# Performance work log

Hardware: AMD Instinct MI355X
Metric: run time of the kernel (lower is better)

The kernel has to match this reference:

```python
import jax, jax.numpy as jnp
from jax import lax
import numpy as np

B, S, E, H, V = 16, 512, 300, 512, 10000


def setup_inputs() -> dict:
    key = jax.random.key(0)
    ks = jax.random.split(key, 7)
    sE = 1.0 / np.sqrt(H)  # torch nn.RNN init scale U(-1/sqrt(H), 1/sqrt(H)); randn*scale is fine for a numeric baseline
    return {
        "x": jax.random.normal(ks[0], (B, S, E), dtype=jnp.float32),
        "W_ih": jax.random.normal(ks[1], (H, E), dtype=jnp.float32) * sE,
        "W_hh": jax.random.normal(ks[2], (H, H), dtype=jnp.float32) * sE,
        "b_ih": jax.random.normal(ks[3], (H,), dtype=jnp.float32) * sE,
        "b_hh": jax.random.normal(ks[4], (H,), dtype=jnp.float32) * sE,
        "W_fc": jax.random.normal(ks[5], (V, H), dtype=jnp.float32) * sE,
        "b_fc": jax.random.normal(ks[6], (V,), dtype=jnp.float32) * sE,
    }


def reference(x, W_ih, W_hh, b_ih, b_hh, W_fc, b_fc):
    # Precompute the input projection for all timesteps: [B,S,H]
    xw = jnp.einsum("bse,he->bsh", x, W_ih) + b_ih + b_hh

    def step(h, xt):
        # h: [B,H], xt: [B,H]
        h = jnp.tanh(xt + h @ W_hh.T)
        return h, h

    h0 = jnp.zeros((x.shape[0], W_hh.shape[0]), dtype=x.dtype)
    _, hs = lax.scan(step, h0, jnp.swapaxes(xw, 0, 1))  # hs: [S,B,H]
    hs = jnp.swapaxes(hs, 0, 1)  # [B,S,H]
    logits = jnp.einsum("bsh,vh->bsv", hs, W_fc) + b_fc  # [B,S,V]
    # Faithful to source: Softmax(dim=1) -> over the SEQUENCE axis
    return jax.nn.softmax(logits, axis=1)
```

## Files before the change

### kernel.cpp

```cpp
#include <hip/hip_runtime.h>
#include <hip/hip_bf16.h>
#include <math.h>

#define B_ 16
#define S_ 512
#define E_ 300
#define H_ 512
#define V_ 10000
#define BS_ (B_ * S_)

#define NSL 16
#define JPB (H_ / NSL)
#define NBLK (B_ * NSL)

typedef __attribute__((ext_vector_type(4))) float f32x4;
typedef __attribute__((ext_vector_type(8))) short bf16x8;
typedef unsigned long long u64;

#define PART_WORDS (4 * B_ * H_)

__global__ __launch_bounds__(256) void k0_init(u64* __restrict__ part) {
  const int idx = blockIdx.x * 256 + threadIdx.x;
  part[idx] = 0xFFFFFFFF00000000ull;
}

__global__ __launch_bounds__(256) void k1_xw(const float* __restrict__ x,
                                             const float* __restrict__ W_ih,
                                             const float* __restrict__ b_ih,
                                             const float* __restrict__ b_hh,
                                             float* __restrict__ xw) {
  __shared__ float As[64][156];
  __shared__ float Ws[64][156];
  const int row0 = blockIdx.x * 64;
  const int col0 = blockIdx.y * 64;
  const int tid = threadIdx.x;
  const int ty = tid >> 4, tx = tid & 15;
  float acc[4][4];
#pragma unroll
  for (int ii = 0; ii < 4; ++ii)
#pragma unroll
    for (int jj = 0; jj < 4; ++jj) acc[ii][jj] = 0.f;

  for (int idx = tid; idx < 64 * 38; idx += 256) {
    const int r = idx / 38, e4 = idx - r * 38;
    *(float4*)&As[r][e4 * 4] =
        *(const float4*)&x[(size_t)(row0 + r) * E_ + e4 * 4];
    *(float4*)&Ws[r][e4 * 4] =
        *(const float4*)&W_ih[(size_t)(col0 + r) * E_ + e4 * 4];
  }
  __syncthreads();
#pragma unroll 2
  for (int e4 = 0; e4 < 38; ++e4) {
    f32x4 a[4], w[4];
#pragma unroll
    for (int ii = 0; ii < 4; ++ii)
      a[ii] = *(const f32x4*)&As[ty + 16 * ii][e4 * 4];
#pragma unroll
    for (int jj = 0; jj < 4; ++jj)
      w[jj] = *(const f32x4*)&Ws[tx + 16 * jj][e4 * 4];
#pragma unroll
    for (int ii = 0; ii < 4; ++ii)
#pragma unroll
      for (int jj = 0; jj < 4; ++jj) {
        const f32x4 p = a[ii] * w[jj];
        acc[ii][jj] += p.x + p.y + p.z + p.w;
      }
  }
  __syncthreads();

  for (int idx = tid; idx < 64 * 37; idx += 256) {
    const int r = idx / 37, e4 = idx - r * 37;
    *(float4*)&As[r][e4 * 4] =
        *(const float4*)&x[(size_t)(row0 + r) * E_ + 152 + e4 * 4];
    *(float4*)&Ws[r][e4 * 4] =
        *(const float4*)&W_ih[(size_t)(col0 + r) * E_ + 152 + e4 * 4];
  }
  __syncthreads();
#pragma unroll 2
  for (int e4 = 0; e4 < 37; ++e4) {
    f32x4 a[4], w[4];
#pragma unroll
    for (int ii = 0; ii < 4; ++ii)
      a[ii] = *(const f32x4*)&As[ty + 16 * ii][e4 * 4];
#pragma unroll
    for (int jj = 0; jj < 4; ++jj)
      w[jj] = *(const f32x4*)&Ws[tx + 16 * jj][e4 * 4];
#pragma unroll
    for (int ii = 0; ii < 4; ++ii)
#pragma unroll
      for (int jj = 0; jj < 4; ++jj) {
        const f32x4 p = a[ii] * w[jj];
        acc[ii][jj] += p.x + p.y + p.z + p.w;
      }
  }

#pragma unroll
  for (int jj = 0; jj < 4; ++jj) {
    const int h = col0 + tx + 16 * jj;
    const float bb = b_ih[h] + b_hh[h];
#pragma unroll
    for (int ii = 0; ii < 4; ++ii)
      xw[(size_t)(row0 + ty + 16 * ii) * H_ + h] = acc[ii][jj] + bb;
  }
}

__device__ __forceinline__ u64 pload(const u64* p) {
  return __hip_atomic_load(p, __ATOMIC_RELAXED, __HIP_MEMORY_SCOPE_AGENT);
}
__device__ __forceinline__ u64 load_sc0(const u64* p) {
  u64 r;
  asm volatile("global_load_dwordx2 %0, %1, off sc0\n\ts_waitcnt vmcnt(0)"
               : "=v"(r) : "v"(p) : "memory");
  return r;
}
__device__ __forceinline__ void store_sc0(u64* p, u64 v) {
  asm volatile("global_store_dwordx2 %0, %1, off sc0" :: "v"(p), "v"(v)
               : "memory");
}

__global__ __launch_bounds__(512) void k2_scan(
    const float* __restrict__ xw, const float* __restrict__ W_hh,
    float* __restrict__ hs, u64* __restrict__ part) {
  const int b = blockIdx.x & 15;
  const int g = blockIdx.x >> 4;
  const int tid = threadIdx.x;
  const int j = tid >> 4;
  const int q = tid & 15;
  const int jg = g * JPB + j;

  __shared__ f32x4 Wp[8 * 512];
  __shared__ f32x4 hp4[2][128];

  {
    const float* wrow = &W_hh[(size_t)jg * H_ + q * 32];
#pragma unroll
    for (int i4 = 0; i4 < 8; ++i4)
      Wp[i4 * 512 + tid] = *(const f32x4*)&wrow[i4 * 4];
  }
  if (tid < 128) hp4[0][tid] = (f32x4)0.f;

  u64* const pf = part + (size_t)b * H_;
  u64* const ps = part + (size_t)(2 * B_ + b) * H_;
  const int kk = ((tid & 63) >> 2) * 32 + (tid >> 6) * 4 + (tid & 3);
  bool fast = true;

  float xwv = xw[(size_t)b * S_ * H_ + jg];
  __syncthreads();

  for (int t = 0; t < S_; ++t) {
    const int cur = t & 1;
    f32x4 a4 = (f32x4)0.f;
#pragma unroll
    for (int i4 = 0; i4 < 8; ++i4) {
      const f32x4 wv = Wp[i4 * 512 + tid];
      const f32x4 hv = hp4[cur][i4 * 16 + q];
      a4 += wv * hv;
    }
    float acc = a4.x + a4.y + a4.z + a4.w;
    acc += __shfl_xor(acc, 1);
    acc += __shfl_xor(acc, 2);
    acc += __shfl_xor(acc, 4);
    acc += __shfl_xor(acc, 8);

    if (q == 0) {
      const float hn = tanhf(xwv + acc);
      const u64 pk =
          ((u64)(unsigned)t << 32) | (u64)(unsigned)__float_as_uint(hn);
      store_sc0(&pf[(size_t)cur * (B_ * H_) + jg], pk);
      __hip_atomic_store(&ps[(size_t)cur * (B_ * H_) + jg], pk,
                         __ATOMIC_RELAXED, __HIP_MEMORY_SCOPE_AGENT);
      hs[((size_t)b * S_ + t) * H_ + jg] = hn;
    }
    const int tn = (t + 1 < S_) ? t + 1 : t;
    const float xw_next = xw[((size_t)b * S_ + tn) * H_ + jg];

    if (t + 1 < S_) {
      u64 v = 0;
      bool got = false;
      const u64* fw = &pf[(size_t)cur * (B_ * H_) + kk];
      if (fast) {
        for (int it = 0; it < 64; ++it) {
          v = load_sc0(fw);
          if ((unsigned)(v >> 32) == (unsigned)t) { got = true; break; }
        }
        if (!got) fast = false;
      }
      if (!got) {
        const u64* sw = &ps[(size_t)cur * (B_ * H_) + kk];
        v = pload(sw);
        while ((unsigned)(v >> 32) != (unsigned)t) v = pload(sw);
      }
      ((float*)&hp4[cur ^ 1][0])[tid] = __uint_as_float((unsigned)v);
    }
    xwv = xw_next;
    __syncthreads();
  }
}

__device__ __forceinline__ unsigned short bf16_rtn(float f) {
  unsigned u = __float_as_uint(f);
  return (unsigned short)((u + 0x7FFFu + ((u >> 16) & 1u)) >> 16);
}
__global__ __launch_bounds__(256) void k5_split(const float* __restrict__ src,
                                                unsigned short* __restrict__ hi,
                                                unsigned short* __restrict__ lo,
                                                int n4) {
  const int i = blockIdx.x * 256 + threadIdx.x;
  if (i >= n4) return;
  const float4 f = *(const float4*)&src[i * 4];
  unsigned short h[4], l[4];
  const float ff[4] = {f.x, f.y, f.z, f.w};
#pragma unroll
  for (int k = 0; k < 4; ++k) {
    h[k] = bf16_rtn(ff[k]);
    const float fh = __uint_as_float((unsigned)h[k] << 16);
    l[k] = bf16_rtn(ff[k] - fh);
  }
  *(ushort4*)&hi[i * 4] = make_ushort4(h[0], h[1], h[2], h[3]);
  *(ushort4*)&lo[i * 4] = make_ushort4(l[0], l[1], l[2], l[3]);
}

__global__ __launch_bounds__(256) void k5_cast(const float* __restrict__ src,
                                               unsigned short* __restrict__ dst,
                                               int n4) {
  const int i = blockIdx.x * 256 + threadIdx.x;
  if (i >= n4) return;
  const float4 f = *(const float4*)&src[i * 4];
  *(ushort4*)&dst[i * 4] = make_ushort4(bf16_rtn(f.x), bf16_rtn(f.y),
                                        bf16_rtn(f.z), bf16_rtn(f.w));
}

__global__ __launch_bounds__(256) void k3_logits(
    const unsigned short* __restrict__ Abg, const unsigned short* __restrict__ Bhg,
    const unsigned short* __restrict__ Blg, const float* __restrict__ b_fc,
    float* __restrict__ out, float2* __restrict__ pstats) {
  __shared__ unsigned short Ab[2][128 * 32];
  __shared__ unsigned short Bh[2][128 * 32];
  __shared__ unsigned short Bl[2][128 * 32];
  __shared__ float2 sstat[2][2][4][16];
  const int m0 = blockIdx.x * 128;
  const int n0 = blockIdx.y * 128;
  const int tid = threadIdx.x;
  const int lane = tid & 63;
  const int wave = tid >> 6;
  const int wm = wave >> 1, wn = wave & 1;
  const int lr = lane & 15;
  const int lg = lane >> 4;
  const int cxr = (lg ^ (lr & 3)) * 8;
  const int lrow = lane >> 2;
  const int lchunk = (lane & 3) ^ (lrow & 3);

  const unsigned short* src[6];
  unsigned short* d0[6];
  unsigned short* d1[6];
#pragma unroll
  for (int t = 0; t < 6; ++t) {
    const int id = wave * 6 + t;
    const int arr = id >> 3;
    const int c16 = id & 7;
    const int r = c16 * 16 + lrow;
    const int grow = (arr == 0) ? (m0 + r) : min(n0 + r, V_ - 1);
    const unsigned short* g = (arr == 0) ? Abg : (arr == 1) ? Bhg : Blg;
    src[t] = g + (size_t)grow * H_ + lchunk * 8;
    unsigned short* l0 = (arr == 0) ? Ab[0] : (arr == 1) ? Bh[0] : Bl[0];
    unsigned short* l1 = (arr == 0) ? Ab[1] : (arr == 1) ? Bh[1] : Bl[1];
    d0[t] = l0 + c16 * 512;
    d1[t] = l1 + c16 * 512;
  }

  f32x4 acc[4][4];
#pragma unroll
  for (int mi = 0; mi < 4; ++mi)
#pragma unroll
    for (int ni = 0; ni < 4; ++ni) acc[mi][ni] = (f32x4)0.0f;

  auto STAGE0 = [&](int k0) {
#pragma unroll
    for (int t = 0; t < 6; ++t)
      __builtin_amdgcn_global_load_lds(
          (const __attribute__((address_space(1))) void*)(src[t] + k0),
          (__attribute__((address_space(3))) void*)d0[t], 16, 0, 0);
  };
  auto STAGE1 = [&](int k0) {
#pragma unroll
    for (int t = 0; t < 6; ++t)
      __builtin_amdgcn_global_load_lds(
          (const __attribute__((address_space(1))) void*)(src[t] + k0),
          (__attribute__((address_space(3))) void*)d1[t], 16, 0, 0);
  };
  auto COMPUTE = [&](int buf) {
    bf16x8 ab[4], bh[4], bl[4];
#pragma unroll
    for (int i = 0; i < 4; ++i) {
      ab[i] = *(const bf16x8*)&Ab[buf][(wm * 64 + i * 16 + lr) * 32 + cxr];
      bh[i] = *(const bf16x8*)&Bh[buf][(wn * 64 + i * 16 + lr) * 32 + cxr];
      bl[i] = *(const bf16x8*)&Bl[buf][(wn * 64 + i * 16 + lr) * 32 + cxr];
    }
#pragma unroll
    for (int mi = 0; mi < 4; ++mi)
#pragma unroll
      for (int ni = 0; ni < 4; ++ni) {
        acc[mi][ni] = __builtin_amdgcn_mfma_f32_16x16x32_bf16(
            ab[mi], bh[ni], acc[mi][ni], 0, 0, 0);
        acc[mi][ni] = __builtin_amdgcn_mfma_f32_16x16x32_bf16(
            ab[mi], bl[ni], acc[mi][ni], 0, 0, 0);
      }
  };

  STAGE0(0);
  __syncthreads();
  for (int kt = 0; kt < 16; kt += 2) {
    STAGE1((kt + 1) * 32);
    COMPUTE(0);
    __syncthreads();
    if (kt + 2 < 16) STAGE0((kt + 2) * 32);
    COMPUTE(1);
    __syncthreads();
  }

#pragma unroll
  for (int ni = 0; ni < 4; ++ni) {
    const int v = n0 + wn * 64 + ni * 16 + lr;
    if (v >= V_) continue;
    const float bias = b_fc[v];
#pragma unroll
    for (int mi = 0; mi < 4; ++mi) {
      const int mrow = m0 + wm * 64 + mi * 16 + lg * 4;
#pragma unroll
      for (int r = 0; r < 4; ++r)
        out[(size_t)(mrow + r) * V_ + v] = acc[mi][ni][r] + bias;
    }
  }

  float pm[4], psum[4];
#pragma unroll
  for (int ni = 0; ni < 4; ++ni) {
    const int v = n0 + wn * 64 + ni * 16 + lr;
    float m = -3.4e38f, s = 0.f;
    if (v < V_) {
      const float bias = b_fc[v];
#pragma unroll
      for (int mi = 0; mi < 4; ++mi)
#pragma unroll
        for (int r = 0; r < 4; ++r)
          m = fmaxf(m, acc[mi][ni][r] + bias);
#pragma unroll
      for (int mi = 0; mi < 4; ++mi)
#pragma unroll
        for (int r = 0; r < 4; ++r)
          s += __expf(acc[mi][ni][r] + bias - m);
    }
#pragma unroll
    for (int d = 16; d <= 32; d <<= 1) {
      const float om = __shfl_xor(m, d);
      const float os = __shfl_xor(s, d);
      const float nm = fmaxf(m, om);
      s = s * __expf(m - nm) + os * __expf(om - nm);
      m = nm;
    }
    pm[ni] = m;
    psum[ni] = s;
  }
  __syncthreads();
  if (lg == 0) {
#pragma unroll
    for (int ni = 0; ni < 4; ++ni)
      sstat[wm][wn][ni][lr] = make_float2(pm[ni], psum[ni]);
  }
  __syncthreads();
  if (wm == 0 && lg == 0) {
#pragma unroll
    for (int ni = 0; ni < 4; ++ni) {
      const int v = n0 + wn * 64 + ni * 16 + lr;
      if (v < V_) {
        const float2 s0 = sstat[0][wn][ni][lr];
        const float2 s1 = sstat[1][wn][ni][lr];
        const float nm = fmaxf(s0.x, s1.x);
        const float ss =
            s0.y * __expf(s0.x - nm) + s1.y * __expf(s1.x - nm);
        pstats[(size_t)blockIdx.x * V_ + v] = make_float2(nm, ss);
      }
    }
  }
}

__global__ __launch_bounds__(256) void k4_merge(const float2* __restrict__ pstats,
                                                float* __restrict__ stats) {
  const int gg = blockIdx.x * 256 + threadIdx.x;
  const int b = gg / V_;
  const int v = gg - b * V_;
  float m = -3.4e38f, s = 0.f;
#pragma unroll
  for (int i = 0; i < 4; ++i) {
    const float2 p = pstats[(size_t)(4 * b + i) * V_ + v];
    const float nm = fmaxf(m, p.x);
    s = s * __expf(m - nm) + p.y * __expf(p.x - nm);
    m = nm;
  }
  stats[2 * gg] = m;
  stats[2 * gg + 1] = 1.f / s;
}

__global__ __launch_bounds__(256) void k4_norm(float* __restrict__ logits,
                                               const float* __restrict__ stats) {
  const int bs = blockIdx.y;
  const int b = bs >> 9;
  const int v0 = blockIdx.x * 2048 + threadIdx.x * 8;
  if (v0 >= V_) return;
  float* p = logits + (size_t)bs * V_ + v0;
  const float* st = stats + 2 * (b * V_ + v0);
  const float4 l0 = *(const float4*)&p[0];
  const float4 l1 = *(const float4*)&p[4];
  const float4 s0 = *(const float4*)&st[0];
  const float4 s1 = *(const float4*)&st[4];
  const float4 s2 = *(const float4*)&st[8];
  const float4 s3 = *(const float4*)&st[12];
  float4 o0, o1;
  o0.x = __expf(l0.x - s0.x) * s0.y;
  o0.y = __expf(l0.y - s0.z) * s0.w;
  o0.z = __expf(l0.z - s1.x) * s1.y;
  o0.w = __expf(l0.w - s1.z) * s1.w;
  o1.x = __expf(l1.x - s2.x) * s2.y;
  o1.y = __expf(l1.y - s2.z) * s2.w;
  o1.z = __expf(l1.z - s3.x) * s3.y;
  o1.w = __expf(l1.w - s3.z) * s3.w;
  *(float4*)&p[0] = o0;
  *(float4*)&p[4] = o1;
}

extern "C" void kernel_launch(void* const* d_in, const int* in_sizes, int n_in,
                              void* d_out, int out_size, void* d_ws,
                              size_t ws_size, hipStream_t stream) {
  const float* x    = (const float*)d_in[0];
  const float* W_ih = (const float*)d_in[1];
  const float* W_hh = (const float*)d_in[2];
  const float* b_ih = (const float*)d_in[3];
  const float* b_hh = (const float*)d_in[4];
  const float* W_fc = (const float*)d_in[5];
  const float* b_fc = (const float*)d_in[6];
  float* out = (float*)d_out;

  float* ws = (float*)d_ws;
  float* xw    = ws;
  float* hs    = xw + (size_t)BS_ * H_;
  float* stats = hs + (size_t)BS_ * H_;
  unsigned short* wfc_hi = (unsigned short*)(stats + (size_t)2 * B_ * V_);
  unsigned short* wfc_lo = wfc_hi + (size_t)V_ * H_;
  float2* pstats = (float2*)(wfc_lo + (size_t)V_ * H_);
  u64* part = (u64*)wfc_hi;
  unsigned short* hs_b = (unsigned short*)xw;

  k0_init<<<PART_WORDS / 256, 256, 0, stream>>>(part);
  k1_xw<<<dim3(BS_ / 64, H_ / 64), 256, 0, stream>>>(x, W_ih, b_ih, b_hh, xw);
  k2_scan<<<NBLK, 512, 0, stream>>>(xw, W_hh, hs, part);
  k5_split<<<((V_ * H_ / 4) + 255) / 256, 256, 0, stream>>>(W_fc, wfc_hi,
                                                            wfc_lo, V_ * H_ / 4);
  k5_cast<<<((BS_ * H_ / 4) + 255) / 256, 256, 0, stream>>>(hs, hs_b,
                                                            BS_ * H_ / 4);
  k3_logits<<<dim3(BS_ / 128, (V_ + 127) / 128), 256, 0, stream>>>(
      hs_b, wfc_hi, wfc_lo, b_fc, out, pstats);
  k4_merge<<<(B_ * V_) / 256, 256, 0, stream>>>(pstats, stats);
  k4_norm<<<dim3((V_ + 2047) / 2048, BS_), 256, 0, stream>>>(out, stats);
}
```

Before: 1.235 ms.

## Fuse softmax normalization into logits GEMM via cross-block stat exchange

```diff
diff --git a/kernel.cpp b/kernel.cpp
--- a/kernel.cpp
+++ b/kernel.cpp
@@ -12,16 +12,20 @@
 #define NSL 16
 #define JPB (H_ / NSL)
 #define NBLK (B_ * NSL)
+#define NT ((V_ + 127) / 128)
 
 typedef __attribute__((ext_vector_type(4))) float f32x4;
 typedef __attribute__((ext_vector_type(8))) short bf16x8;
 typedef unsigned long long u64;
 
 #define PART_WORDS (4 * B_ * H_)
-
-__global__ __launch_bounds__(256) void k0_init(u64* __restrict__ part) {
+#define STAT_WORDS (64 * NT * 128)
+
+__global__ __launch_bounds__(256) void k0_init(u64* __restrict__ part,
+                                               u64* __restrict__ statmb) {
   const int idx = blockIdx.x * 256 + threadIdx.x;
-  part[idx] = 0xFFFFFFFF00000000ull;
+  if (idx < PART_WORDS) part[idx] = 0xFFFFFFFF00000000ull;
+  if (idx < STAT_WORDS) statmb[idx] = 0xFFC00000FFC00000ull;
 }
 
 __global__ __launch_bounds__(256) void k1_xw(const float* __restrict__ x,
@@ -233,11 +237,12 @@
 __global__ __launch_bounds__(256) void k3_logits(
     const unsigned short* __restrict__ Abg, const unsigned short* __restrict__ Bhg,
     const unsigned short* __restrict__ Blg, const float* __restrict__ b_fc,
-    float* __restrict__ out, float2* __restrict__ pstats) {
+    float* __restrict__ out, u64* __restrict__ statmb) {
   __shared__ unsigned short Ab[2][128 * 32];
   __shared__ unsigned short Bh[2][128 * 32];
   __shared__ unsigned short Bl[2][128 * 32];
   __shared__ float2 sstat[2][2][4][16];
+  __shared__ float2 fstat[128];
   const int m0 = blockIdx.x * 128;
   const int n0 = blockIdx.y * 128;
   const int tid = threadIdx.x;
@@ -318,20 +323,6 @@
     __syncthreads();
   }
 
-#pragma unroll
-  for (int ni = 0; ni < 4; ++ni) {
-    const int v = n0 + wn * 64 + ni * 16 + lr;
-    if (v >= V_) continue;
-    const float bias = b_fc[v];
-#pragma unroll
-    for (int mi = 0; mi < 4; ++mi) {
-      const int mrow = m0 + wm * 64 + mi * 16 + lg * 4;
-#pragma unroll
-      for (int r = 0; r < 4; ++r)
-        out[(size_t)(mrow + r) * V_ + v] = acc[mi][ni][r] + bias;
-    }
-  }
-
   float pm[4], psum[4];
 #pragma unroll
   for (int ni = 0; ni < 4; ++ni) {
@@ -368,64 +359,60 @@
       sstat[wm][wn][ni][lr] = make_float2(pm[ni], psum[ni]);
   }
   __syncthreads();
-  if (wm == 0 && lg == 0) {
+
+  if (wave < 2 && lg == 0) {
+    const int base = (int)(blockIdx.x & ~3u);
+    float bm[4], bs[4];
 #pragma unroll
     for (int ni = 0; ni < 4; ++ni) {
-      const int v = n0 + wn * 64 + ni * 16 + lr;
-      if (v < V_) {
-        const float2 s0 = sstat[0][wn][ni][lr];
-        const float2 s1 = sstat[1][wn][ni][lr];
-        const float nm = fmaxf(s0.x, s1.x);
-        const float ss =
-            s0.y * __expf(s0.x - nm) + s1.y * __expf(s1.x - nm);
-        pstats[(size_t)blockIdx.x * V_ + v] = make_float2(nm, ss);
-      }
-    }
-  }
-}
-
-__global__ __launch_bounds__(256) void k4_merge(const float2* __restrict__ pstats,
-                                                float* __restrict__ stats) {
-  const int gg = blockIdx.x * 256 + threadIdx.x;
-  const int b = gg / V_;
-  const int v = gg - b * V_;
-  float m = -3.4e38f, s = 0.f;
-#pragma unroll
-  for (int i = 0; i < 4; ++i) {
-    const float2 p = pstats[(size_t)(4 * b + i) * V_ + v];
-    const float nm = fmaxf(m, p.x);
-    s = s * __expf(m - nm) + p.y * __expf(p.x - nm);
-    m = nm;
-  }
-  stats[2 * gg] = m;
-  stats[2 * gg + 1] = 1.f / s;
-}
-
-__global__ __launch_bounds__(256) void k4_norm(float* __restrict__ logits,
-                                               const float* __restrict__ stats) {
-  const int bs = blockIdx.y;
-  const int b = bs >> 9;
-  const int v0 = blockIdx.x * 2048 + threadIdx.x * 8;
-  if (v0 >= V_) return;
-  float* p = logits + (size_t)bs * V_ + v0;
-  const float* st = stats + 2 * (b * V_ + v0);
-  const float4 l0 = *(const float4*)&p[0];
-  const float4 l1 = *(const float4*)&p[4];
-  const float4 s0 = *(const float4*)&st[0];
-  const float4 s1 = *(const float4*)&st[4];
-  const float4 s2 = *(const float4*)&st[8];
-  const float4 s3 = *(const float4*)&st[12];
-  float4 o0, o1;
-  o0.x = __expf(l0.x - s0.x) * s0.y;
-  o0.y = __expf(l0.y - s0.z) * s0.w;
-  o0.z = __expf(l0.z - s1.x) * s1.y;
-  o0.w = __expf(l0.w - s1.z) * s1.w;
-  o1.x = __expf(l1.x - s2.x) * s2.y;
-  o1.y = __expf(l1.y - s2.z) * s2.w;
-  o1.z = __expf(l1.z - s3.x) * s3.y;
-  o1.w = __expf(l1.w - s3.z) * s3.w;
-  *(float4*)&p[0] = o0;
-  *(float4*)&p[4] = o1;
+      const int col = wn * 64 + ni * 16 + lr;
+      const float2 s0 = sstat[0][wn][ni][lr];
+      const float2 s1 = sstat[1][wn][ni][lr];
+      const float nm = fmaxf(s0.x, s1.x);
+      bm[ni] = nm;
+      bs[ni] = s0.y * __expf(s0.x - nm) + s1.y * __expf(s1.x - nm);
+      const u64 pk = ((u64)(unsigned)__float_as_uint(bm[ni]) << 32) |
+                     (u64)(unsigned)__float_as_uint(bs[ni]);
+      __hip_atomic_store(
+          &statmb[((size_t)blockIdx.x * NT + blockIdx.y) * 128 + col], pk,
+          __ATOMIC_RELAXED, __HIP_MEMORY_SCOPE_AGENT);
+    }
+#pragma unroll
+    for (int ni = 0; ni < 4; ++ni) {
+      const int col = wn * 64 + ni * 16 + lr;
+      float M = bm[ni], S = bs[ni];
+      for (int i = 0; i < 4; ++i) {
+        const int pb = base + i;
+        if (pb == (int)blockIdx.x) continue;
+        const u64* w = &statmb[((size_t)pb * NT + blockIdx.y) * 128 + col];
+        u64 v = pload(w);
+        while ((unsigned)(v >> 32) == 0xFFC00000u) v = pload(w);
+        const float om = __uint_as_float((unsigned)(v >> 32));
+        const float os = __uint_as_float((unsigned)v);
+        const float nm = fmaxf(M, om);
+        S = S * __expf(M - nm) + os * __expf(om - nm);
+        M = nm;
+      }
+      fstat[col] = make_float2(M, 1.f / S);
+    }
+  }
+  __syncthreads();
+
+#pragma unroll
+  for (int ni = 0; ni < 4; ++ni) {
+    const int v = n0 + wn * 64 + ni * 16 + lr;
+    if (v >= V_) continue;
+    const float bias = b_fc[v];
+    const float2 fs = fstat[wn * 64 + ni * 16 + lr];
+#pragma unroll
+    for (int mi = 0; mi < 4; ++mi) {
+      const int mrow = m0 + wm * 64 + mi * 16 + lg * 4;
+#pragma unroll
+      for (int r = 0; r < 4; ++r)
+        out[(size_t)(mrow + r) * V_ + v] =
+            __expf(acc[mi][ni][r] + bias - fs.x) * fs.y;
+    }
+  }
 }
 
 extern "C" void kernel_launch(void* const* d_in, const int* in_sizes, int n_in,
@@ -443,22 +430,19 @@
   float* ws = (float*)d_ws;
   float* xw    = ws;
   float* hs    = xw + (size_t)BS_ * H_;
-  float* stats = hs + (size_t)BS_ * H_;
-  unsigned short* wfc_hi = (unsigned short*)(stats + (size_t)2 * B_ * V_);
+  unsigned short* wfc_hi = (unsigned short*)(hs + (size_t)BS_ * H_);
   unsigned short* wfc_lo = wfc_hi + (size_t)V_ * H_;
-  float2* pstats = (float2*)(wfc_lo + (size_t)V_ * H_);
+  u64* statmb = (u64*)(wfc_lo + (size_t)V_ * H_);
   u64* part = (u64*)wfc_hi;
   unsigned short* hs_b = (unsigned short*)xw;
 
-  k0_init<<<PART_WORDS / 256, 256, 0, stream>>>(part);
+  k0_init<<<(STAT_WORDS + 255) / 256, 256, 0, stream>>>(part, statmb);
   k1_xw<<<dim3(BS_ / 64, H_ / 64), 256, 0, stream>>>(x, W_ih, b_ih, b_hh, xw);
   k2_scan<<<NBLK, 512, 0, stream>>>(xw, W_hh, hs, part);
   k5_split<<<((V_ * H_ / 4) + 255) / 256, 256, 0, stream>>>(W_fc, wfc_hi,
                                                             wfc_lo, V_ * H_ / 4);
   k5_cast<<<((BS_ * H_ / 4) + 255) / 256, 256, 0, stream>>>(hs, hs_b,
                                                             BS_ * H_ / 4);
-  k3_logits<<<dim3(BS_ / 128, (V_ + 127) / 128), 256, 0, stream>>>(
-      hs_b, wfc_hi, wfc_lo, b_fc, out, pstats);
-  k4_merge<<<(B_ * V_) / 256, 256, 0, stream>>>(pstats, stats);
-  k4_norm<<<dim3((V_ + 2047) / 2048, BS_), 256, 0, stream>>>(out, stats);
-}
+  k3_logits<<<dim3(BS_ / 128, NT), 256, 0, stream>>>(hs_b, wfc_hi, wfc_lo,
+                                                     b_fc, out, statmb);
+}
```

After: 1.104 ms. -10.6%, faster.
